# Kernel optimization log

Measured on AMD Instinct MI355X. Metric: run time of the kernel, lower is better.

## Reference

```python
import jax, jax.numpy as jnp
import numpy as np

N_HEAD = 16
NEG = 1e10


def setup_inputs() -> dict:
    key = jax.random.key(0)
    k1, k2, k3 = jax.random.split(key, 3)
    nx = 1024
    B, S = 2, 2048
    x = jax.random.normal(k1, (B, S, nx), dtype=jnp.float32)
    w_attn = jax.random.normal(k2, (nx, 3 * nx), dtype=jnp.float32) * (1.0 / np.sqrt(nx))
    b_attn = jnp.zeros((3 * nx,), dtype=jnp.float32)
    w_proj = jax.random.normal(k3, (nx, nx), dtype=jnp.float32) * (1.0 / np.sqrt(nx))
    b_proj = jnp.zeros((nx,), dtype=jnp.float32)
    return {"x": x, "w_attn": w_attn, "b_attn": b_attn, "w_proj": w_proj, "b_proj": b_proj}


def reference(x, w_attn, b_attn, w_proj, b_proj):
    B, S, nx = x.shape
    d = nx // N_HEAD
    qkv = x @ w_attn + b_attn                      # [B,S,3*nx]
    q, k, v = jnp.split(qkv, 3, axis=-1)
    # split heads: [B,S,nx] -> [B,H,S,d]
    q = q.reshape(B, S, N_HEAD, d).transpose(0, 2, 1, 3)
    k = k.reshape(B, S, N_HEAD, d).transpose(0, 2, 1, 3)
    v = v.reshape(B, S, N_HEAD, d).transpose(0, 2, 1, 3)
    # present: stack of (key stored as [B,H,S,d], value) like torch code
    present = jnp.stack((k, v))                    # [2,B,H,S,d]
    # scores with scale and additive causal mask (GPT-2 style: w*b - 1e10*(1-b))
    w = jnp.einsum('bhqd,bhkd->bhqk', q, k) / jnp.sqrt(jnp.float32(d))
    mask = jnp.tril(jnp.ones((S, S), dtype=w.dtype))[None, None]
    w = w * mask - NEG * (1.0 - mask)
    w = jax.nn.softmax(w, axis=-1)
    a = jnp.einsum('bhqk,bhkd->bhqd', w, v)        # [B,H,S,d]
    a = a.transpose(0, 2, 1, 3).reshape(B, S, nx)  # merge heads
    a = a @ w_proj + b_proj
    return (a, present)
```

## Files before the change

### kernel.cpp

```cpp
#include <hip/hip_runtime.h>
#include <stdint.h>
#include <stddef.h>

#define DEVI __device__ __forceinline__

typedef __bf16 bf16x8 __attribute__((ext_vector_type(8)));
typedef float  f32x4  __attribute__((ext_vector_type(4)));
typedef float  f32x16 __attribute__((ext_vector_type(16)));
typedef unsigned short u16;
typedef uint32_t u32;
typedef u16 u16x8 __attribute__((ext_vector_type(8)));
typedef u16 u16x4 __attribute__((ext_vector_type(4)));
typedef u32 u32x2 __attribute__((ext_vector_type(2)));
typedef u32 u32x4 __attribute__((ext_vector_type(4)));

typedef __attribute__((address_space(1))) void as1_void;
typedef __attribute__((address_space(3))) void as3_void;

static constexpr float SC = 0.18033688011112042f;

DEVI u16 f2bf(float f) {
  uint32_t u = __builtin_bit_cast(uint32_t, f);
  u += 0x7fffu + ((u >> 16) & 1u);
  return (u16)(u >> 16);
}

DEVI void gload_lds16(const void* g, void* l) {
  __builtin_amdgcn_global_load_lds((as1_void*)(void*)g, (as3_void*)l, 16, 0, 0);
}

#if __has_builtin(__builtin_amdgcn_exp2f)
DEVI float fast_exp2(float x) { return __builtin_amdgcn_exp2f(x); }
#else
DEVI float fast_exp2(float x) { return exp2f(x); }
#endif

DEVI u32 cvtpk(float lo, float hi) {
  u32 r;
  asm("v_cvt_pk_bf16_f32 %0, %1, %2" : "=v"(r) : "v"(lo), "v"(hi));
  return r;
}
DEVI void plswap(u32& a, u32& b) {
  asm("v_permlane32_swap_b32 %0, %1" : "+v"(a), "+v"(b));
}

__global__ __launch_bounds__(256) void k_cvt(const float* __restrict__ in,
                                             u16* __restrict__ out, int n) {
  int i = (blockIdx.x * 256 + threadIdx.x) * 4;
  if (i >= n) return;
  const float4 v = *(const float4*)(in + i);
  u16x4 o = { f2bf(v.x), f2bf(v.y), f2bf(v.z), f2bf(v.w) };
  *(u16x4*)(out + i) = o;
}

__global__ __launch_bounds__(256) void k_tcvt(const float* __restrict__ in,
                                              u16* __restrict__ out, int R, int C) {
  __shared__ float tile[32][33];
  const int c0 = blockIdx.x * 32, r0 = blockIdx.y * 32;
  const int tx = threadIdx.x, ty = threadIdx.y;
#pragma unroll
  for (int i = ty; i < 32; i += 8)
    tile[i][tx] = in[(size_t)(r0 + i) * C + (c0 + tx)];
  __syncthreads();
#pragma unroll
  for (int i = ty; i < 32; i += 8)
    out[(size_t)(c0 + i) * R + (r0 + tx)] = f2bf(tile[tx][i]);
}

template <int EPI>
__global__ __launch_bounds__(256) void k_gemm(
    const u16* __restrict__ A, const u16* __restrict__ Bt,
    const float* __restrict__ bias,
    u16* __restrict__ wq, u16* __restrict__ wk, u16* __restrict__ vt,
    float* __restrict__ pk, float* __restrict__ pv, float* __restrict__ of) {
  constexpr int K = 1024;
  __shared__ __align__(16) u16 Ash[2][128 * 32];
  __shared__ __align__(16) u16 Bsh[2][128 * 32];
  const int tid = threadIdx.x;
  const int lane = tid & 63, wid = tid >> 6;
  const int wm = wid >> 1, wn = wid & 1;
  const int lr = lane & 15, lg = lane >> 4;
  const int m0 = blockIdx.y * 128, n0 = blockIdx.x * 128;

  const int c = wid * 64 + lane;
  const u16* Ag1 = A + (size_t)(m0 + (c >> 2)) * K + (c & 3) * 8;
  const u16* Ag2 = A + (size_t)(m0 + 64 + (c >> 2)) * K + (c & 3) * 8;
  const u16* Bg1 = Bt + (size_t)(n0 + (c >> 2)) * K + (c & 3) * 8;
  const u16* Bg2 = Bt + (size_t)(n0 + 64 + (c >> 2)) * K + (c & 3) * 8;

  f32x4 acc[4][4];
#pragma unroll
  for (int i = 0; i < 4; ++i)
#pragma unroll
    for (int j = 0; j < 4; ++j) acc[i][j] = (f32x4)0.0f;

#define STAGE(sel, kk)                                        \
  {                                                           \
    gload_lds16(Ag1 + (kk), &Ash[sel][wid * 512]);            \
    gload_lds16(Ag2 + (kk), &Ash[sel][2048 + wid * 512]);     \
    gload_lds16(Bg1 + (kk), &Bsh[sel][wid * 512]);            \
    gload_lds16(Bg2 + (kk), &Bsh[sel][2048 + wid * 512]);     \
  }

  STAGE(0, 0)
  __syncthreads();
  int cur = 0;
  for (int k0 = 0; k0 < K; k0 += 32) {
    if (k0 + 32 < K) STAGE(cur ^ 1, k0 + 32)
    bf16x8 af[4], bfr[4];
#pragma unroll
    for (int f = 0; f < 4; ++f) {
      af[f]  = *(const bf16x8*)&Ash[cur][(wm * 64 + f * 16 + lr) * 32 + lg * 8];
      bfr[f] = *(const bf16x8*)&Bsh[cur][(wn * 64 + f * 16 + lr) * 32 + lg * 8];
    }
#pragma unroll
    for (int i = 0; i < 4; ++i)
#pragma unroll
      for (int j = 0; j < 4; ++j)
        acc[i][j] = __builtin_amdgcn_mfma_f32_16x16x32_bf16(af[i], bfr[j], acc[i][j], 0, 0, 0);
    __syncthreads();
    cur ^= 1;
  }
#undef STAGE

  if constexpr (EPI == 0) {
#pragma unroll
    for (int j = 0; j < 4; ++j) {
      const int n = n0 + wn * 64 + j * 16 + lr;
      const float bv = bias[n];
      const int sec = n >> 10;
      const int nn = n & 1023;
      const int h = nn >> 6, dd = nn & 63;
#pragma unroll
      for (int i = 0; i < 4; ++i) {
        const int mb = m0 + wm * 64 + i * 16 + lg * 4;
        const int bb = mb >> 11, ss = mb & 2047;
        const size_t ib = (size_t)(bb * 16 + h) * 131072 + (size_t)ss * 64 + dd;
        if (sec == 0) {
#pragma unroll
          for (int r = 0; r < 4; ++r)
            wq[ib + (size_t)r * 64] = f2bf(acc[i][j][r] + bv);
        } else if (sec == 1) {
#pragma unroll
          for (int r = 0; r < 4; ++r) {
            const float v = acc[i][j][r] + bv;
            wk[ib + (size_t)r * 64] = f2bf(v);
            pk[ib + (size_t)r * 64] = v;
          }
        } else {
          u16x4 vv;
#pragma unroll
          for (int r = 0; r < 4; ++r) {
            const float v = acc[i][j][r] + bv;
            pv[ib + (size_t)r * 64] = v;
            vv[r] = f2bf(v);
          }
          *(u16x4*)(vt + ((size_t)(bb * 16 + h) * 64 + dd) * 2048 + ss) = vv;
        }
      }
    }
  } else {
#pragma unroll
    for (int j = 0; j < 4; ++j) {
      const int n = n0 + wn * 64 + j * 16 + lr;
      const float bv = bias[n];
#pragma unroll
      for (int i = 0; i < 4; ++i) {
        const int mb = m0 + wm * 64 + i * 16 + lg * 4;
#pragma unroll
        for (int r = 0; r < 4; ++r)
          of[(size_t)(mb + r) * 1024 + n] = acc[i][j][r] + bv;
      }
    }
  }
}

__global__ __launch_bounds__(128) void k_attn(const u16* __restrict__ Q,
                                              const u16* __restrict__ Kp,
                                              const u16* __restrict__ VT,
                                              u16* __restrict__ AO) {
  __shared__ __align__(16) u16 Ksh[2][4096];
  __shared__ __align__(16) u16 Vsh[2][4096];

  const int tid = threadIdx.x;
  const int lane = tid & 63, w = tid >> 6;
  const int l31 = lane & 31, hi = lane >> 5;
  const int bid = blockIdx.x;
  const int bh = bid & 31;
  const int qt = 31 - (bid >> 5);
  const int b = bh >> 4, h = bh & 15;
  const size_t hb = (size_t)bh * (2048 * 64);

  const int T = qt + 1;
  const int qb = qt * 64 + w * 32;

  const int srow = w * 32 + (lane >> 3);
  const int sslot = (lane & 7) ^ (lane >> 3);
  const u16* Kg = Kp + hb + (size_t)srow * 64 + sslot * 8;
  const u16* Vg = VT + hb + (size_t)srow * 2048 + sslot * 8;

#define STAGEA(sel, jt)                                                       \
  {                                                                           \
    gload_lds16(Kg + (size_t)(jt) * 4096,          &Ksh[sel][w * 2048]);      \
    gload_lds16(Kg + (size_t)(jt) * 4096 + 512,    &Ksh[sel][w * 2048 + 512]);\
    gload_lds16(Kg + (size_t)(jt) * 4096 + 1024,   &Ksh[sel][w * 2048 + 1024]);\
    gload_lds16(Kg + (size_t)(jt) * 4096 + 1536,   &Ksh[sel][w * 2048 + 1536]);\
    gload_lds16(Vg + (size_t)(jt) * 64,            &Vsh[sel][w * 2048]);      \
    gload_lds16(Vg + (size_t)(jt) * 64 + 16384,    &Vsh[sel][w * 2048 + 512]);\
    gload_lds16(Vg + (size_t)(jt) * 64 + 32768,    &Vsh[sel][w * 2048 + 1024]);\
    gload_lds16(Vg + (size_t)(jt) * 64 + 49152,    &Vsh[sel][w * 2048 + 1536]);\
  }

  const u16* Qp = Q + hb + (size_t)(qb + l31) * 64 + hi * 8;
  const bf16x8 qf0 = *(const bf16x8*)(Qp);
  const bf16x8 qf1 = *(const bf16x8*)(Qp + 16);
  const bf16x8 qf2 = *(const bf16x8*)(Qp + 32);
  const bf16x8 qf3 = *(const bf16x8*)(Qp + 48);

  f32x16 o0 = (f32x16)0.0f, o1 = (f32x16)0.0f;
  float mrun = -1e30f, lrun = 0.0f;

  const int xr = l31 & 7;

  STAGEA(0, 0)
  __syncthreads();
  int sel = 0;
  for (int jt = 0; jt < T; ++jt) {
    if (jt + 1 < T) STAGEA(sel ^ 1, jt + 1)
    const u16* Kb = Ksh[sel];
    const u16* Vb = Vsh[sel];
    bf16x8 kf[2][4];
#pragma unroll
    for (int s = 0; s < 2; ++s)
#pragma unroll
      for (int c = 0; c < 4; ++c)
        kf[s][c] = *(const bf16x8*)&Kb[(s * 32 + l31) * 64 + (((2 * c + hi) ^ xr) * 8)];

    f32x16 s0 = (f32x16)0.0f, s1 = (f32x16)0.0f;
    __builtin_amdgcn_s_setprio(1);
    s0 = __builtin_amdgcn_mfma_f32_32x32x16_bf16(kf[0][0], qf0, s0, 0, 0, 0);
    s1 = __builtin_amdgcn_mfma_f32_32x32x16_bf16(kf[1][0], qf0, s1, 0, 0, 0);
    s0 = __builtin_amdgcn_mfma_f32_32x32x16_bf16(kf[0][1], qf1, s0, 0, 0, 0);
    s1 = __builtin_amdgcn_mfma_f32_32x32x16_bf16(kf[1][1], qf1, s1, 0, 0, 0);
    s0 = __builtin_amdgcn_mfma_f32_32x32x16_bf16(kf[0][2], qf2, s0, 0, 0, 0);
    s1 = __builtin_amdgcn_mfma_f32_32x32x16_bf16(kf[1][2], qf2, s1, 0, 0, 0);
    s0 = __builtin_amdgcn_mfma_f32_32x32x16_bf16(kf[0][3], qf3, s0, 0, 0, 0);
    s1 = __builtin_amdgcn_mfma_f32_32x32x16_bf16(kf[1][3], qf3, s1, 0, 0, 0);
    __builtin_amdgcn_s_setprio(0);

    if (jt == T - 1) {
      const int qrel = w * 32 + l31;
      const int h4 = hi * 4;
#pragma unroll
      for (int r = 0; r < 16; ++r) {
        const int kp = (r & 3) + ((r >> 2) << 3) + h4;
        s0[r] = (kp <= qrel) ? s0[r] : -1e30f;
        s1[r] = (kp + 32 <= qrel) ? s1[r] : -1e30f;
      }
    }

    float t8[8];
#pragma unroll
    for (int r = 0; r < 8; ++r)
      t8[r] = fmaxf(fmaxf(s0[r], s0[r + 8]), fmaxf(s1[r], s1[r + 8]));
    float tm = fmaxf(fmaxf(fmaxf(t8[0], t8[1]), fmaxf(t8[2], t8[3])),
                     fmaxf(fmaxf(t8[4], t8[5]), fmaxf(t8[6], t8[7])));
    tm = fmaxf(tm, __shfl_xor(tm, 32));
    if (!__all(tm <= mrun)) {
      const float mnew = fmaxf(mrun, tm);
      const float al = fast_exp2((mrun - mnew) * SC);
      mrun = mnew;
      lrun *= al;
#pragma unroll
      for (int r = 0; r < 16; ++r) { o0[r] *= al; o1[r] *= al; }
    }
    const float nb = -mrun * SC;
#pragma unroll
    for (int r = 0; r < 16; ++r) {
      s0[r] = fast_exp2(fmaf(s0[r], SC, nb));
      s1[r] = fast_exp2(fmaf(s1[r], SC, nb));
    }
    float u8[8];
#pragma unroll
    for (int r = 0; r < 8; ++r)
      u8[r] = (s0[r] + s0[r + 8]) + (s1[r] + s1[r + 8]);
    lrun += ((u8[0] + u8[1]) + (u8[2] + u8[3])) + ((u8[4] + u8[5]) + (u8[6] + u8[7]));

    bf16x8 pb0, pb1, pb2, pb3;
#define PACK_CHUNK(sv, bb, dst)                                   \
    {                                                             \
      u32 a0 = cvtpk(sv[bb + 0], sv[bb + 1]);                     \
      u32 a1 = cvtpk(sv[bb + 2], sv[bb + 3]);                     \
      u32 a2 = cvtpk(sv[bb + 4], sv[bb + 5]);                     \
      u32 a3 = cvtpk(sv[bb + 6], sv[bb + 7]);                     \
      plswap(a0, a2);                                             \
      plswap(a1, a3);                                             \
      u32x4 fv = {a0, a1, a2, a3};                                \
      dst = __builtin_bit_cast(bf16x8, fv);                       \
    }
    PACK_CHUNK(s0, 0, pb0)
    PACK_CHUNK(s0, 8, pb1)
    PACK_CHUNK(s1, 0, pb2)
    PACK_CHUNK(s1, 8, pb3)
#undef PACK_CHUNK

    bf16x8 vf[2][4];
#pragma unroll
    for (int mt = 0; mt < 2; ++mt)
#pragma unroll
      for (int c = 0; c < 4; ++c)
        vf[mt][c] = *(const bf16x8*)&Vb[(mt * 32 + l31) * 64 + (((2 * c + hi) ^ xr) * 8)];

    __builtin_amdgcn_s_setprio(1);
    o0 = __builtin_amdgcn_mfma_f32_32x32x16_bf16(vf[0][0], pb0, o0, 0, 0, 0);
    o1 = __builtin_amdgcn_mfma_f32_32x32x16_bf16(vf[1][0], pb0, o1, 0, 0, 0);
    o0 = __builtin_amdgcn_mfma_f32_32x32x16_bf16(vf[0][1], pb1, o0, 0, 0, 0);
    o1 = __builtin_amdgcn_mfma_f32_32x32x16_bf16(vf[1][1], pb1, o1, 0, 0, 0);
    o0 = __builtin_amdgcn_mfma_f32_32x32x16_bf16(vf[0][2], pb2, o0, 0, 0, 0);
    o1 = __builtin_amdgcn_mfma_f32_32x32x16_bf16(vf[1][2], pb2, o1, 0, 0, 0);
    o0 = __builtin_amdgcn_mfma_f32_32x32x16_bf16(vf[0][3], pb3, o0, 0, 0, 0);
    o1 = __builtin_amdgcn_mfma_f32_32x32x16_bf16(vf[1][3], pb3, o1, 0, 0, 0);
    __builtin_amdgcn_s_setprio(0);

    __syncthreads();
    sel ^= 1;
  }
#undef STAGEA

  const float lt = lrun + __shfl_xor(lrun, 32);
  const float inv = 1.0f / lt;
  u16* aorow = AO + (size_t)(b * 2048 + qb + l31) * 1024 + h * 64 + hi * 4;
#pragma unroll
  for (int g = 0; g < 4; ++g) {
    u32 w0 = cvtpk(o0[4 * g + 0] * inv, o0[4 * g + 1] * inv);
    u32 w1 = cvtpk(o0[4 * g + 2] * inv, o0[4 * g + 3] * inv);
    u32x2 ww = {w0, w1};
    *(u32x2*)(aorow + g * 8) = ww;
  }
#pragma unroll
  for (int g = 0; g < 4; ++g) {
    u32 w0 = cvtpk(o1[4 * g + 0] * inv, o1[4 * g + 1] * inv);
    u32 w1 = cvtpk(o1[4 * g + 2] * inv, o1[4 * g + 3] * inv);
    u32x2 ww = {w0, w1};
    *(u32x2*)(aorow + 32 + g * 8) = ww;
  }
}

extern "C" void kernel_launch(void* const* d_in, const int* in_sizes, int n_in,
                              void* d_out, int out_size, void* d_ws, size_t ws_size,
                              hipStream_t stream) {
  const float* x      = (const float*)d_in[0];
  const float* w_attn = (const float*)d_in[1];
  const float* b_attn = (const float*)d_in[2];
  const float* w_proj = (const float*)d_in[3];
  const float* b_proj = (const float*)d_in[4];
  float* out = (float*)d_out;

  char* ws = (char*)d_ws;
  u16* x_bf  = (u16*)(ws);
  u16* wat_t = (u16*)(ws + 8388608);
  u16* wpj_t = (u16*)(ws + 14680064);
  u16* q_ws  = (u16*)(ws + 16777216);
  u16* k_ws  = (u16*)(ws + 25165824);
  u16* vT_ws = (u16*)(ws + 33554432);
  u16* a_ws  = (u16*)(ws + 41943040);

  k_cvt<<<4096, 256, 0, stream>>>(x, x_bf, 4194304);
  k_tcvt<<<dim3(96, 32), dim3(32, 8), 0, stream>>>(w_attn, wat_t, 1024, 3072);
  k_tcvt<<<dim3(32, 32), dim3(32, 8), 0, stream>>>(w_proj, wpj_t, 1024, 1024);

  k_gemm<0><<<dim3(24, 32), 256, 0, stream>>>(x_bf, wat_t, b_attn,
                                              q_ws, k_ws, vT_ws,
                                              out + 4194304, out + 8388608, nullptr);

  k_attn<<<dim3(1024), 128, 0, stream>>>(q_ws, k_ws, vT_ws, a_ws);

  k_gemm<1><<<dim3(8, 32), 256, 0, stream>>>(a_ws, wpj_t, b_proj,
                                             nullptr, nullptr, nullptr,
                                             nullptr, nullptr, out);
}
```

Measured before the change: 131.9 us.

## Triple-buffer attention K/V loads, reorder causal tiles, move V transpose to separate kernel

The attention kernel moves from double to triple buffering of K/V tiles. It prefetches two tiles ahead and waits with an explicit vmcnt count plus a raw s_barrier instead of __syncthreads, so more global loads overlap with compute. Query tiles are assigned in an interleaved heavy/light order to balance causal work across the 1024 blocks. The QKV GEMM epilogue now writes V in row-major layout, and a new small kernel transposes it into a reused workspace slot, replacing the scattered strided V^T stores. The cost is an extra kernel launch, an extra pass over V, and more LDS per attention block.

```diff
diff --git a/kernel.cpp b/kernel.cpp
--- a/kernel.cpp
+++ b/kernel.cpp
@@ -67,11 +67,37 @@
     out[(size_t)(c0 + i) * R + (r0 + tx)] = f2bf(tile[tx][i]);
 }
 
+__global__ __launch_bounds__(256) void k_vt(const u16* __restrict__ in,
+                                            u16* __restrict__ out) {
+  __shared__ u16 tile[64][72];
+  const int tid = threadIdx.x;
+  const int s0 = blockIdx.x * 64;
+  const int bh = blockIdx.y;
+  const size_t ib = (size_t)bh * 131072;
+#pragma unroll
+  for (int it = 0; it < 2; ++it) {
+    const int r = (tid >> 3) + it * 32;
+    const int c8 = (tid & 7) * 8;
+    u16x8 v = *(const u16x8*)(in + ib + (size_t)(s0 + r) * 64 + c8);
+    *(u16x8*)&tile[r][c8] = v;
+  }
+  __syncthreads();
+#pragma unroll
+  for (int it = 0; it < 2; ++it) {
+    const int d = (tid >> 3) + it * 32;
+    const int s8 = (tid & 7) * 8;
+    u16x8 v;
+#pragma unroll
+    for (int jj = 0; jj < 8; ++jj) v[jj] = tile[s8 + jj][d];
+    *(u16x8*)(out + ib + (size_t)d * 2048 + s0 + s8) = v;
+  }
+}
+
 template <int EPI>
 __global__ __launch_bounds__(256) void k_gemm(
     const u16* __restrict__ A, const u16* __restrict__ Bt,
     const float* __restrict__ bias,
-    u16* __restrict__ wq, u16* __restrict__ wk, u16* __restrict__ vt,
+    u16* __restrict__ wq, u16* __restrict__ wk, u16* __restrict__ wv,
     float* __restrict__ pk, float* __restrict__ pv, float* __restrict__ of) {
   constexpr int K = 1024;
   __shared__ __align__(16) u16 Ash[2][128 * 32];
@@ -148,14 +174,12 @@
             pk[ib + (size_t)r * 64] = v;
           }
         } else {
-          u16x4 vv;
 #pragma unroll
           for (int r = 0; r < 4; ++r) {
             const float v = acc[i][j][r] + bv;
+            wv[ib + (size_t)r * 64] = f2bf(v);
             pv[ib + (size_t)r * 64] = v;
-            vv[r] = f2bf(v);
           }
-          *(u16x4*)(vt + ((size_t)(bb * 16 + h) * 64 + dd) * 2048 + ss) = vv;
         }
       }
     }
@@ -179,15 +203,17 @@
                                               const u16* __restrict__ Kp,
                                               const u16* __restrict__ VT,
                                               u16* __restrict__ AO) {
-  __shared__ __align__(16) u16 Ksh[2][4096];
-  __shared__ __align__(16) u16 Vsh[2][4096];
+  __shared__ __align__(16) u16 Ksh[3][4096];
+  __shared__ __align__(16) u16 Vsh[3][4096];
 
   const int tid = threadIdx.x;
   const int lane = tid & 63, w = tid >> 6;
   const int l31 = lane & 31, hi = lane >> 5;
   const int bid = blockIdx.x;
   const int bh = bid & 31;
-  const int qt = 31 - (bid >> 5);
+  const int j4 = bid >> 8;
+  const int g  = (bid >> 5) & 7;
+  const int qt = (j4 == 0) ? (31 - g) : (j4 == 1) ? g : (j4 == 2) ? (23 - g) : (8 + g);
   const int b = bh >> 4, h = bh & 15;
   const size_t hb = (size_t)bh * (2048 * 64);
 
@@ -223,12 +249,23 @@
   const int xr = l31 & 7;
 
   STAGEA(0, 0)
-  __syncthreads();
-  int sel = 0;
+  if (T > 1) {
+    STAGEA(1, 1)
+    asm volatile("s_waitcnt vmcnt(8)" ::: "memory");
+  } else {
+    asm volatile("s_waitcnt vmcnt(0)" ::: "memory");
+  }
+  __builtin_amdgcn_sched_barrier(0);
+  __builtin_amdgcn_s_barrier();
+  __builtin_amdgcn_sched_barrier(0);
+
+  int cur = 0;
   for (int jt = 0; jt < T; ++jt) {
-    if (jt + 1 < T) STAGEA(sel ^ 1, jt + 1)
-    const u16* Kb = Ksh[sel];
-    const u16* Vb = Vsh[sel];
+    const bool pf = (jt + 2 < T);
+    int nb = cur + 2; if (nb >= 3) nb -= 3;
+    if (pf) STAGEA(nb, jt + 2)
+    const u16* Kb = Ksh[cur];
+    const u16* Vb = Vsh[cur];
     bf16x8 kf[2][4];
 #pragma unroll
     for (int s = 0; s < 2; ++s)
@@ -274,11 +311,11 @@
 #pragma unroll
       for (int r = 0; r < 16; ++r) { o0[r] *= al; o1[r] *= al; }
     }
-    const float nb = -mrun * SC;
+    const float nb2 = -mrun * SC;
 #pragma unroll
     for (int r = 0; r < 16; ++r) {
-      s0[r] = fast_exp2(fmaf(s0[r], SC, nb));
-      s1[r] = fast_exp2(fmaf(s1[r], SC, nb));
+      s0[r] = fast_exp2(fmaf(s0[r], SC, nb2));
+      s1[r] = fast_exp2(fmaf(s1[r], SC, nb2));
     }
     float u8[8];
 #pragma unroll
@@ -322,8 +359,12 @@
     o1 = __builtin_amdgcn_mfma_f32_32x32x16_bf16(vf[1][3], pb3, o1, 0, 0, 0);
     __builtin_amdgcn_s_setprio(0);
 
-    __syncthreads();
-    sel ^= 1;
+    if (pf) asm volatile("s_waitcnt vmcnt(8)" ::: "memory");
+    else    asm volatile("s_waitcnt vmcnt(0)" ::: "memory");
+    __builtin_amdgcn_sched_barrier(0);
+    __builtin_amdgcn_s_barrier();
+    __builtin_amdgcn_sched_barrier(0);
+    cur = (cur + 1 == 3) ? 0 : cur + 1;
   }
 #undef STAGEA
 
@@ -331,18 +372,18 @@
   const float inv = 1.0f / lt;
   u16* aorow = AO + (size_t)(b * 2048 + qb + l31) * 1024 + h * 64 + hi * 4;
 #pragma unroll
-  for (int g = 0; g < 4; ++g) {
-    u32 w0 = cvtpk(o0[4 * g + 0] * inv, o0[4 * g + 1] * inv);
-    u32 w1 = cvtpk(o0[4 * g + 2] * inv, o0[4 * g + 3] * inv);
+  for (int g2 = 0; g2 < 4; ++g2) {
+    u32 w0 = cvtpk(o0[4 * g2 + 0] * inv, o0[4 * g2 + 1] * inv);
+    u32 w1 = cvtpk(o0[4 * g2 + 2] * inv, o0[4 * g2 + 3] * inv);
     u32x2 ww = {w0, w1};
-    *(u32x2*)(aorow + g * 8) = ww;
-  }
-#pragma unroll
-  for (int g = 0; g < 4; ++g) {
-    u32 w0 = cvtpk(o1[4 * g + 0] * inv, o1[4 * g + 1] * inv);
-    u32 w1 = cvtpk(o1[4 * g + 2] * inv, o1[4 * g + 3] * inv);
+    *(u32x2*)(aorow + g2 * 8) = ww;
+  }
+#pragma unroll
+  for (int g2 = 0; g2 < 4; ++g2) {
+    u32 w0 = cvtpk(o1[4 * g2 + 0] * inv, o1[4 * g2 + 1] * inv);
+    u32 w1 = cvtpk(o1[4 * g2 + 2] * inv, o1[4 * g2 + 3] * inv);
     u32x2 ww = {w0, w1};
-    *(u32x2*)(aorow + 32 + g * 8) = ww;
+    *(u32x2*)(aorow + 32 + g2 * 8) = ww;
   }
 }
 
@@ -362,16 +403,19 @@
   u16* wpj_t = (u16*)(ws + 14680064);
   u16* q_ws  = (u16*)(ws + 16777216);
   u16* k_ws  = (u16*)(ws + 25165824);
-  u16* vT_ws = (u16*)(ws + 33554432);
+  u16* v_ws  = (u16*)(ws + 33554432);
   u16* a_ws  = (u16*)(ws + 41943040);
+  u16* vT_ws = (u16*)(ws);
 
   k_cvt<<<4096, 256, 0, stream>>>(x, x_bf, 4194304);
   k_tcvt<<<dim3(96, 32), dim3(32, 8), 0, stream>>>(w_attn, wat_t, 1024, 3072);
   k_tcvt<<<dim3(32, 32), dim3(32, 8), 0, stream>>>(w_proj, wpj_t, 1024, 1024);
 
   k_gemm<0><<<dim3(24, 32), 256, 0, stream>>>(x_bf, wat_t, b_attn,
-                                              q_ws, k_ws, vT_ws,
+                                              q_ws, k_ws, v_ws,
                                               out + 4194304, out + 8388608, nullptr);
+
+  k_vt<<<dim3(32, 32), 256, 0, stream>>>(v_ws, vT_ws);
 
   k_attn<<<dim3(1024), 128, 0, stream>>>(q_ws, k_ws, vT_ws, a_ws);
 
```

New measurement: 140.5 us. 6.5% more time.

## Triple-buffer GEMM prefetch with vmcnt waits, XCD block swizzle, balanced attention tile order

Applied to the files above, without the earlier changes.

The GEMM now uses three LDS stages and prefetches two K-tiles ahead. It replaces __syncthreads with explicit vmcnt waits plus s_barrier, and raises wave priority around the MFMAs. Workgroup IDs are remapped so that consecutive blocks land on the same XCD for L2 reuse. The attention kernel reorders causal query tiles in a zigzag to balance heavy and light tiles across dispatch waves. These changes add LDS use (lower occupancy risk) and rely on hand-tuned wait counts being correct.

```diff
diff --git a/kernel.cpp b/kernel.cpp
--- a/kernel.cpp
+++ b/kernel.cpp
@@ -74,13 +74,19 @@
     u16* __restrict__ wq, u16* __restrict__ wk, u16* __restrict__ vt,
     float* __restrict__ pk, float* __restrict__ pv, float* __restrict__ of) {
   constexpr int K = 1024;
-  __shared__ __align__(16) u16 Ash[2][128 * 32];
-  __shared__ __align__(16) u16 Bsh[2][128 * 32];
+  constexpr int NT = K / 32;
+  __shared__ __align__(16) u16 Ash[3][128 * 32];
+  __shared__ __align__(16) u16 Bsh[3][128 * 32];
   const int tid = threadIdx.x;
   const int lane = tid & 63, wid = tid >> 6;
   const int wm = wid >> 1, wn = wid & 1;
   const int lr = lane & 15, lg = lane >> 4;
-  const int m0 = blockIdx.y * 128, n0 = blockIdx.x * 128;
+
+  const int nwgx = gridDim.x;
+  const int nwg = nwgx * gridDim.y;
+  int lbid = blockIdx.y * nwgx + blockIdx.x;
+  lbid = (lbid & 7) * (nwg >> 3) + (lbid >> 3);
+  const int m0 = (lbid / nwgx) * 128, n0 = (lbid % nwgx) * 128;
 
   const int c = wid * 64 + lane;
   const u16* Ag1 = A + (size_t)(m0 + (c >> 2)) * K + (c & 3) * 8;
@@ -103,23 +109,36 @@
   }
 
   STAGE(0, 0)
-  __syncthreads();
+  STAGE(1, 32)
+  asm volatile("s_waitcnt vmcnt(4)" ::: "memory");
+  __builtin_amdgcn_sched_barrier(0);
+  __builtin_amdgcn_s_barrier();
+  __builtin_amdgcn_sched_barrier(0);
+
   int cur = 0;
-  for (int k0 = 0; k0 < K; k0 += 32) {
-    if (k0 + 32 < K) STAGE(cur ^ 1, k0 + 32)
+  for (int j = 0; j < NT; ++j) {
+    const bool pf = (j + 2 < NT);
+    int nb = cur + 2; if (nb >= 3) nb -= 3;
+    if (pf) STAGE(nb, (j + 2) * 32)
     bf16x8 af[4], bfr[4];
 #pragma unroll
     for (int f = 0; f < 4; ++f) {
       af[f]  = *(const bf16x8*)&Ash[cur][(wm * 64 + f * 16 + lr) * 32 + lg * 8];
       bfr[f] = *(const bf16x8*)&Bsh[cur][(wn * 64 + f * 16 + lr) * 32 + lg * 8];
     }
+    __builtin_amdgcn_s_setprio(1);
 #pragma unroll
     for (int i = 0; i < 4; ++i)
 #pragma unroll
-      for (int j = 0; j < 4; ++j)
-        acc[i][j] = __builtin_amdgcn_mfma_f32_16x16x32_bf16(af[i], bfr[j], acc[i][j], 0, 0, 0);
-    __syncthreads();
-    cur ^= 1;
+      for (int jj = 0; jj < 4; ++jj)
+        acc[i][jj] = __builtin_amdgcn_mfma_f32_16x16x32_bf16(af[i], bfr[jj], acc[i][jj], 0, 0, 0);
+    __builtin_amdgcn_s_setprio(0);
+    if (pf) asm volatile("s_waitcnt vmcnt(4)" ::: "memory");
+    else    asm volatile("s_waitcnt vmcnt(0)" ::: "memory");
+    __builtin_amdgcn_sched_barrier(0);
+    __builtin_amdgcn_s_barrier();
+    __builtin_amdgcn_sched_barrier(0);
+    cur = (cur + 1 == 3) ? 0 : cur + 1;
   }
 #undef STAGE
 
@@ -187,7 +206,9 @@
   const int l31 = lane & 31, hi = lane >> 5;
   const int bid = blockIdx.x;
   const int bh = bid & 31;
-  const int qt = 31 - (bid >> 5);
+  const int j4 = bid >> 8;
+  const int g  = (bid >> 5) & 7;
+  const int qt = (j4 == 0) ? (31 - g) : (j4 == 1) ? g : (j4 == 2) ? (23 - g) : (8 + g);
   const int b = bh >> 4, h = bh & 15;
   const size_t hb = (size_t)bh * (2048 * 64);
 
@@ -224,6 +245,7 @@
 
   STAGEA(0, 0)
   __syncthreads();
+
   int sel = 0;
   for (int jt = 0; jt < T; ++jt) {
     if (jt + 1 < T) STAGEA(sel ^ 1, jt + 1)
@@ -274,11 +296,11 @@
 #pragma unroll
       for (int r = 0; r < 16; ++r) { o0[r] *= al; o1[r] *= al; }
     }
-    const float nb = -mrun * SC;
+    const float nb2 = -mrun * SC;
 #pragma unroll
     for (int r = 0; r < 16; ++r) {
-      s0[r] = fast_exp2(fmaf(s0[r], SC, nb));
-      s1[r] = fast_exp2(fmaf(s1[r], SC, nb));
+      s0[r] = fast_exp2(fmaf(s0[r], SC, nb2));
+      s1[r] = fast_exp2(fmaf(s1[r], SC, nb2));
     }
     float u8[8];
 #pragma unroll
@@ -331,18 +353,18 @@
   const float inv = 1.0f / lt;
   u16* aorow = AO + (size_t)(b * 2048 + qb + l31) * 1024 + h * 64 + hi * 4;
 #pragma unroll
-  for (int g = 0; g < 4; ++g) {
-    u32 w0 = cvtpk(o0[4 * g + 0] * inv, o0[4 * g + 1] * inv);
-    u32 w1 = cvtpk(o0[4 * g + 2] * inv, o0[4 * g + 3] * inv);
+  for (int g2 = 0; g2 < 4; ++g2) {
+    u32 w0 = cvtpk(o0[4 * g2 + 0] * inv, o0[4 * g2 + 1] * inv);
+    u32 w1 = cvtpk(o0[4 * g2 + 2] * inv, o0[4 * g2 + 3] * inv);
     u32x2 ww = {w0, w1};
-    *(u32x2*)(aorow + g * 8) = ww;
-  }
-#pragma unroll
-  for (int g = 0; g < 4; ++g) {
-    u32 w0 = cvtpk(o1[4 * g + 0] * inv, o1[4 * g + 1] * inv);
-    u32 w1 = cvtpk(o1[4 * g + 2] * inv, o1[4 * g + 3] * inv);
+    *(u32x2*)(aorow + g2 * 8) = ww;
+  }
+#pragma unroll
+  for (int g2 = 0; g2 < 4; ++g2) {
+    u32 w0 = cvtpk(o1[4 * g2 + 0] * inv, o1[4 * g2 + 1] * inv);
+    u32 w1 = cvtpk(o1[4 * g2 + 2] * inv, o1[4 * g2 + 3] * inv);
     u32x2 ww = {w0, w1};
-    *(u32x2*)(aorow + 32 + g * 8) = ww;
+    *(u32x2*)(aorow + 32 + g2 * 8) = ww;
   }
 }
 
```

Result: slower. 150.2 us (+13.9%).
